# Performance work log

Measured on AMD Instinct MI355X. Metric: run time of the kernel, lower is better.

The kernel has to match this reference:

```python
import jax, jax.numpy as jnp
import numpy as np

B, T, I, H, O = 256, 2048, 6, 64, 6  # batch, time, input_dim, hidden_dim, output_dim


def setup_inputs() -> dict:
    key = jax.random.key(0)
    ks = jax.random.split(key, 11)
    s = 0.1  # param init scale
    return {
        "x": jax.random.normal(ks[0], (B, T, I), jnp.float32),
        # LSTM layer 0 (gate order i, f, g, o as in PyTorch; b = b_ih + b_hh)
        "Wih0": jax.random.normal(ks[1], (4 * H, I), jnp.float32) * s,
        "Whh0": jax.random.normal(ks[2], (4 * H, H), jnp.float32) * s,
        "b0": jax.random.normal(ks[3], (4 * H,), jnp.float32) * s,
        # LSTM layer 1
        "Wih1": jax.random.normal(ks[4], (4 * H, H), jnp.float32) * s,
        "Whh1": jax.random.normal(ks[5], (4 * H, H), jnp.float32) * s,
        "b1": jax.random.normal(ks[6], (4 * H,), jnp.float32) * s,
        # FC head
        "W1": jax.random.normal(ks[7], (H, H), jnp.float32) * s,
        "bf1": jax.random.normal(ks[8], (H,), jnp.float32) * s,
        "W2": jax.random.normal(ks[9], (O, H), jnp.float32) * s,
        "bf2": jax.random.normal(ks[10], (O,), jnp.float32) * s,
    }


def lstm_layer(x, Wih, Whh, b):
    """Single LSTM layer, batch_first. x: (B, T, F) -> (B, T, H)."""
    h_dim = Whh.shape[1]
    # precompute input contribution to gates for all timesteps: (B, T, 4H)
    xg = jnp.einsum('btf,gf->btg', x, Wih) + b

    def step(carry, xg_t):
        h, c = carry
        g = xg_t + h @ Whh.T                      # (B, 4H)
        i, f, gg, o = jnp.split(g, 4, axis=-1)    # PyTorch gate order i,f,g,o
        i = jax.nn.sigmoid(i)
        f = jax.nn.sigmoid(f)
        gg = jnp.tanh(gg)
        o = jax.nn.sigmoid(o)
        c = f * c + i * gg
        h = o * jnp.tanh(c)
        return (h, c), h

    h0 = jnp.zeros((x.shape[0], h_dim), x.dtype)
    _, hs = jax.lax.scan(step, (h0, h0), jnp.swapaxes(xg, 0, 1))  # (T, B, H)
    return jnp.swapaxes(hs, 0, 1)


def reference(x, Wih0, Whh0, b0, Wih1, Whh1, b1, W1, bf1, W2, bf2):
    h = lstm_layer(x, Wih0, Whh0, b0)
    h = lstm_layer(h, Wih1, Whh1, b1)   # eval mode: inter-layer dropout disabled
    h = jax.nn.relu(h @ W1.T + bf1)
    return h @ W2.T + bf2               # (B, T, O)
```

## Files before the change

### kernel.cpp

```cpp
#include <hip/hip_runtime.h>

#define TT 2048
#define HH 64
#define II 6
#define OO 6
#define NTHR 512

typedef float    f32x4 __attribute__((ext_vector_type(4)));
typedef _Float16 f16x8 __attribute__((ext_vector_type(8)));

__device__ __forceinline__ float fast_sig(float v) {
    return __builtin_amdgcn_rcpf(1.0f + __expf(-v));
}
__device__ __forceinline__ float fast_tanh(float v) {
    return 1.0f - 2.0f * __builtin_amdgcn_rcpf(__expf(2.0f * v) + 1.0f);
}

#define MFMA(a, b, c) __builtin_amdgcn_mfma_f32_16x16x32_f16((a), (b), (c), 0, 0, 0)

__global__
__attribute__((amdgpu_flat_work_group_size(NTHR, NTHR)))
__attribute__((amdgpu_waves_per_eu(2, 2)))
void lstm_mfma_kernel(const float* __restrict__ x,
                      const float* __restrict__ Wih0, const float* __restrict__ Whh0,
                      const float* __restrict__ b0,
                      const float* __restrict__ Wih1, const float* __restrict__ Whh1,
                      const float* __restrict__ b1,
                      const float* __restrict__ W1, const float* __restrict__ bf1,
                      const float* __restrict__ W2, const float* __restrict__ bf2,
                      float* __restrict__ out)
{
    const int row  = blockIdx.x;
    const int tid  = threadIdx.x;
    const int wid  = tid >> 6;
    const int lane = tid & 63;
    const int n    = lane & 15;
    const int q    = lane >> 4;
    const bool isA = wid < 4;
    const int  w   = isA ? wid : wid - 4;

    __shared__ __attribute__((aligned(16))) _Float16 H0[2][HH];
    __shared__ __attribute__((aligned(16))) _Float16 H1[2][HH];
    __shared__ __attribute__((aligned(16))) _Float16 Rb[2][HH];
    __shared__ __attribute__((aligned(16))) _Float16 Xb[2][32];
    __shared__ __attribute__((aligned(16))) float    XG[2][256];

    if (tid < HH) {
        H0[0][tid] = (_Float16)0.f; H0[1][tid] = (_Float16)0.f;
        H1[0][tid] = (_Float16)0.f; H1[1][tid] = (_Float16)0.f;
        Rb[0][tid] = (_Float16)0.f; Rb[1][tid] = (_Float16)0.f;
    }
    if (tid < 32) { Xb[0][tid] = (_Float16)0.f; Xb[1][tid] = (_Float16)0.f; }
    if (tid < 256) { XG[0][tid] = 0.f; XG[1][tid] = 0.f; }

    f16x8 frag[20];
    float bias[8];
    #pragma unroll
    for (int i = 0; i < 8; ++i) bias[i] = 0.f;

    auto mk = [&](const float* W, int r, int ld, int kbase, int kmax, bool rok) {
        f16x8 f;
        #pragma unroll
        for (int i = 0; i < 8; ++i) {
            int kk = kbase + 8 * q + i;
            f[i] = (rok && kk < kmax) ? (_Float16)W[r * ld + kk] : (_Float16)0.f;
        }
        return f;
    };

    if (isA) {
        #pragma unroll
        for (int g = 0; g < 4; ++g) {
            const int r0 = g * HH + 16 * w + n;
            frag[g * 3 + 0] = mk(Whh0, r0, HH, 0,  HH, true);
            frag[g * 3 + 1] = mk(Whh0, r0, HH, 32, HH, true);
            frag[g * 3 + 2] = mk(Wih0, r0, II, 0,  II, true);
            bias[g] = b0[r0];
            const int r1 = 16 * (4 * g + w) + n;
            frag[12 + g * 2 + 0] = mk(Wih1, r1, HH, 0,  HH, true);
            frag[12 + g * 2 + 1] = mk(Wih1, r1, HH, 32, HH, true);
            bias[4 + g] = b1[r1];
        }
    } else {
        #pragma unroll
        for (int g = 0; g < 4; ++g) {
            const int r0 = g * HH + 16 * w + n;
            frag[g * 2 + 0] = mk(Whh1, r0, HH, 0,  HH, true);
            frag[g * 2 + 1] = mk(Whh1, r0, HH, 32, HH, true);
        }
        const int rf = 16 * w + n;
        frag[8]  = mk(W1, rf, HH, 0,  HH, true);
        frag[9]  = mk(W1, rf, HH, 32, HH, true);
        bias[0] = bf1[rf];
        frag[10] = mk(W2, n, HH, 0,  HH, n < OO);
        frag[11] = mk(W2, n, HH, 32, HH, n < OO);
        bias[1] = (n < OO) ? bf2[n] : 0.f;
        #pragma unroll
        for (int i = 12; i < 20; ++i) frag[i] = frag[0];
    }

    const float* xrow   = x   + (size_t)row * TT * II;
    float*       outrow = out + (size_t)row * TT * OO;

    if (tid < II) Xb[0][tid] = (_Float16)xrow[tid];

    float cst = 0.f;
    __syncthreads();

    for (int t = 0; t <= TT + 3; ++t) {
        const int slp = (t + 1) & 1;
        const int slc = t & 1;

        if (isA) {
            const f16x8 a0 = *reinterpret_cast<const f16x8*>(&H0[slp][8 * q]);
            const f16x8 a1 = *reinterpret_cast<const f16x8*>(&H0[slp][32 + 8 * q]);
            const f16x8 a2 = *reinterpret_cast<const f16x8*>(&Xb[slc][8 * q]);
            f32x4 d0, d1, d2, d3;
            #pragma unroll
            for (int g = 0; g < 4; ++g) {
                f32x4 acc = {bias[g], bias[g], bias[g], bias[g]};
                acc = MFMA(a0, frag[g * 3 + 0], acc);
                acc = MFMA(a1, frag[g * 3 + 1], acc);
                acc = MFMA(a2, frag[g * 3 + 2], acc);
                if (g == 0) d0 = acc; else if (g == 1) d1 = acc;
                else if (g == 2) d2 = acc; else d3 = acc;
                f32x4 ae = {bias[4 + g], bias[4 + g], bias[4 + g], bias[4 + g]};
                ae = MFMA(a0, frag[12 + g * 2 + 0], ae);
                ae = MFMA(a1, frag[12 + g * 2 + 1], ae);
                if (lane < 16) XG[slp][16 * (4 * g + w) + lane] = ae[0];
            }
            if (t < TT) {
                float i_ = fast_sig(d0[0]), f_ = fast_sig(d1[0]);
                float g_ = fast_tanh(d2[0]), o_ = fast_sig(d3[0]);
                cst = f_ * cst + i_ * g_;
                float h = o_ * fast_tanh(cst);
                if (lane < 16) H0[slc][16 * w + lane] = (_Float16)h;
            }
            if (wid == 0 && lane < II && t + 1 < TT)
                Xb[slp][lane] = (_Float16)xrow[(size_t)(t + 1) * II + lane];
        } else {
            const int s2 = t - 2, s3 = t - 3, s4 = t - 4;
            const f16x8 a0 = *reinterpret_cast<const f16x8*>(&H1[slp][8 * q]);
            const f16x8 a1 = *reinterpret_cast<const f16x8*>(&H1[slp][32 + 8 * q]);
            f32x4 d0, d1, d2, d3;
            #pragma unroll
            for (int g = 0; g < 4; ++g) {
                const float xg = XG[slc][16 * (4 * g + w) + n];
                f32x4 acc = {xg, xg, xg, xg};
                acc = MFMA(a0, frag[g * 2 + 0], acc);
                acc = MFMA(a1, frag[g * 2 + 1], acc);
                if (g == 0) d0 = acc; else if (g == 1) d1 = acc;
                else if (g == 2) d2 = acc; else d3 = acc;
            }
            if (s2 >= 0 && s2 < TT) {
                float i_ = fast_sig(d0[0]), f_ = fast_sig(d1[0]);
                float g_ = fast_tanh(d2[0]), o_ = fast_sig(d3[0]);
                cst = f_ * cst + i_ * g_;
                float h = o_ * fast_tanh(cst);
                if (lane < 16) H1[slc][16 * w + lane] = (_Float16)h;
            }
            {
                f32x4 acc = {bias[0], bias[0], bias[0], bias[0]};
                acc = MFMA(a0, frag[8], acc);
                acc = MFMA(a1, frag[9], acc);
                if (s3 >= 0 && s3 < TT && lane < 16)
                    Rb[slp][16 * w + lane] = (_Float16)fmaxf(acc[0], 0.f);
            }
            if (w == 0) {
                const f16x8 r0 = *reinterpret_cast<const f16x8*>(&Rb[slc][8 * q]);
                const f16x8 r1 = *reinterpret_cast<const f16x8*>(&Rb[slc][32 + 8 * q]);
                f32x4 acc = {bias[1], bias[1], bias[1], bias[1]};
                acc = MFMA(r0, frag[10], acc);
                acc = MFMA(r1, frag[11], acc);
                if (s4 >= 0 && s4 < TT && lane < OO)
                    outrow[(size_t)s4 * OO + lane] = acc[0];
            }
        }
        __syncthreads();
    }
}

extern "C" void kernel_launch(void* const* d_in, const int* in_sizes, int n_in,
                              void* d_out, int out_size, void* d_ws, size_t ws_size,
                              hipStream_t stream) {
    const float* xp   = (const float*)d_in[0];
    const float* Wih0 = (const float*)d_in[1];
    const float* Whh0 = (const float*)d_in[2];
    const float* b0   = (const float*)d_in[3];
    const float* Wih1 = (const float*)d_in[4];
    const float* Whh1 = (const float*)d_in[5];
    const float* b1   = (const float*)d_in[6];
    const float* W1   = (const float*)d_in[7];
    const float* bf1  = (const float*)d_in[8];
    const float* W2   = (const float*)d_in[9];
    const float* bf2  = (const float*)d_in[10];
    float* outp = (float*)d_out;

    lstm_mfma_kernel<<<dim3(256), dim3(NTHR), 0, stream>>>(
        xp, Wih0, Whh0, b0, Wih1, Whh1, b1, W1, bf1, W2, bf2, outp);
}
```

Before: 1.215 ms.

## Batch 16 rows per block and split LSTM layers across producer/consumer blocks

Replaces the one-row-per-block kernel with 32 blocks: 16 producer blocks run layer 0 for 16 batch rows each and stream h0 through a global ring buffer to 16 consumer blocks that run layer 1 and the FC head. Batching 16 rows fills the MFMA N dimension instead of wasting 15 of 16 columns, and splitting the layers makes each block's per-step critical path shorter. Input projections are computed one step ahead by separate waves. The cost is cross-block spin-wait synchronization through global atomics, a memset of the workspace, and only 32 blocks on the device, so per-step latency dominates.

```diff
diff --git a/kernel.cpp b/kernel.cpp
--- a/kernel.cpp
+++ b/kernel.cpp
@@ -4,10 +4,16 @@
 #define HH 64
 #define II 6
 #define OO 6
+#define MB 16
+#define NG 16
+#define RING 256
 #define NTHR 512
 
 typedef float    f32x4 __attribute__((ext_vector_type(4)));
+typedef float    f32x2 __attribute__((ext_vector_type(2)));
 typedef _Float16 f16x8 __attribute__((ext_vector_type(8)));
+typedef _Float16 f16x4 __attribute__((ext_vector_type(4)));
+typedef _Float16 f16x2 __attribute__((ext_vector_type(2)));
 
 __device__ __forceinline__ float fast_sig(float v) {
     return __builtin_amdgcn_rcpf(1.0f + __expf(-v));
@@ -17,46 +23,47 @@
 }
 
 #define MFMA(a, b, c) __builtin_amdgcn_mfma_f32_16x16x32_f16((a), (b), (c), 0, 0, 0)
+#define LGKM_BARRIER() asm volatile("s_waitcnt lgkmcnt(0)\ns_barrier" ::: "memory")
 
 __global__
 __attribute__((amdgpu_flat_work_group_size(NTHR, NTHR)))
 __attribute__((amdgpu_waves_per_eu(2, 2)))
-void lstm_mfma_kernel(const float* __restrict__ x,
+void lstm_pipe_kernel(const float* __restrict__ x,
                       const float* __restrict__ Wih0, const float* __restrict__ Whh0,
                       const float* __restrict__ b0,
                       const float* __restrict__ Wih1, const float* __restrict__ Whh1,
                       const float* __restrict__ b1,
                       const float* __restrict__ W1, const float* __restrict__ bf1,
                       const float* __restrict__ W2, const float* __restrict__ bf2,
-                      float* __restrict__ out)
+                      float* __restrict__ out, void* __restrict__ ws)
 {
-    const int row  = blockIdx.x;
+    const int bid  = blockIdx.x;
+    const bool isP = bid < NG;
+    const int g    = isP ? bid : bid - NG;
+    const int row0 = g * MB;
     const int tid  = threadIdx.x;
     const int wid  = tid >> 6;
     const int lane = tid & 63;
     const int n    = lane & 15;
     const int q    = lane >> 4;
-    const bool isA = wid < 4;
-    const int  w   = isA ? wid : wid - 4;
-
-    __shared__ __attribute__((aligned(16))) _Float16 H0[2][HH];
-    __shared__ __attribute__((aligned(16))) _Float16 H1[2][HH];
-    __shared__ __attribute__((aligned(16))) _Float16 Rb[2][HH];
-    __shared__ __attribute__((aligned(16))) _Float16 Xb[2][32];
-    __shared__ __attribute__((aligned(16))) float    XG[2][256];
-
-    if (tid < HH) {
-        H0[0][tid] = (_Float16)0.f; H0[1][tid] = (_Float16)0.f;
-        H1[0][tid] = (_Float16)0.f; H1[1][tid] = (_Float16)0.f;
-        Rb[0][tid] = (_Float16)0.f; Rb[1][tid] = (_Float16)0.f;
-    }
-    if (tid < 32) { Xb[0][tid] = (_Float16)0.f; Xb[1][tid] = (_Float16)0.f; }
-    if (tid < 256) { XG[0][tid] = 0.f; XG[1][tid] = 0.f; }
-
-    f16x8 frag[20];
-    float bias[8];
-    #pragma unroll
-    for (int i = 0; i < 8; ++i) bias[i] = 0.f;
+
+    int* p0p = (int*)ws + (size_t)g * 64;
+    int* c0p = (int*)ws + (size_t)(NG + g) * 64;
+    _Float16* ring = (_Float16*)((char*)ws + 65536) + (size_t)g * (RING * 1024);
+
+    __shared__ __attribute__((aligned(16))) _Float16 H0 [4][1024];
+    __shared__ __attribute__((aligned(16))) _Float16 XT [2][128];
+    __shared__ __attribute__((aligned(16))) float    XG0[2][4][4][64][4];
+    __shared__ __attribute__((aligned(16))) _Float16 H0G[4][1024];
+    __shared__ __attribute__((aligned(16))) _Float16 H1 [2][1024];
+    __shared__ __attribute__((aligned(16))) _Float16 Rb [2][1024];
+    __shared__ __attribute__((aligned(16))) float    XG1[2][4][4][64][4];
+
+    for (int i = tid; i < 4 * 1024; i += NTHR) { H0[0][i] = (_Float16)0.f;
+                                                 H0G[0][i] = (_Float16)0.f; }
+    for (int i = tid; i < 2 * 1024; i += NTHR) { H1[0][i] = (_Float16)0.f;
+                                                 Rb[0][i]  = (_Float16)0.f; }
+    if (tid < 2 * 128) XT[0][tid] = (_Float16)0.f;
 
     auto mk = [&](const float* W, int r, int ld, int kbase, int kmax, bool rok) {
         f16x8 f;
@@ -67,116 +74,295 @@
         }
         return f;
     };
-
-    if (isA) {
+    const f32x4 zero4 = {0.f, 0.f, 0.f, 0.f};
+    f16x8 zero8;
+    #pragma unroll
+    for (int i = 0; i < 8; ++i) zero8[i] = (_Float16)0.f;
+
+    f16x8 FR[16];
+    f32x4 B[8];
+    #pragma unroll
+    for (int i = 0; i < 16; ++i) FR[i] = zero8;
+    #pragma unroll
+    for (int i = 0; i < 8; ++i) B[i] = zero4;
+
+    if (isP) {
+        if (wid < 4) {
+            #pragma unroll
+            for (int gg = 0; gg < 4; ++gg) {
+                const int r0 = gg * HH + 16 * wid + n;
+                FR[2 * gg + 0] = mk(Whh0, r0, HH, 0,  HH, true);
+                FR[2 * gg + 1] = mk(Whh0, r0, HH, 32, HH, true);
+            }
+        } else if (wid < 6) {
+            const int j = wid - 4;
+            #pragma unroll
+            for (int ti = 0; ti < 2; ++ti)
+                #pragma unroll
+                for (int gg = 0; gg < 4; ++gg) {
+                    const int tau = 2 * j + ti;
+                    FR[ti * 4 + gg] = mk(Wih0, gg * HH + 16 * tau + n, II, 0, II, true);
+                    const int u0 = gg * HH + 16 * tau + 4 * q;
+                    B[ti * 4 + gg] = f32x4{b0[u0], b0[u0+1], b0[u0+2], b0[u0+3]};
+                }
+        }
+    } else {
+        if (wid < 4) {
+            #pragma unroll
+            for (int gg = 0; gg < 4; ++gg) {
+                const int r0 = gg * HH + 16 * wid + n;
+                FR[2 * gg + 0] = mk(Whh1, r0, HH, 0,  HH, true);
+                FR[2 * gg + 1] = mk(Whh1, r0, HH, 32, HH, true);
+            }
+        } else if (wid < 6) {
+            const int j = wid - 4;
+            #pragma unroll
+            for (int ti = 0; ti < 2; ++ti)
+                #pragma unroll
+                for (int gg = 0; gg < 4; ++gg) {
+                    const int tau = 2 * j + ti;
+                    const int r0 = gg * HH + 16 * tau + n;
+                    FR[(ti * 4 + gg) * 2 + 0] = mk(Wih1, r0, HH, 0,  HH, true);
+                    FR[(ti * 4 + gg) * 2 + 1] = mk(Wih1, r0, HH, 32, HH, true);
+                    const int u0 = gg * HH + 16 * tau + 4 * q;
+                    B[ti * 4 + gg] = f32x4{b1[u0], b1[u0+1], b1[u0+2], b1[u0+3]};
+                }
+        } else if (wid == 7) {
+            #pragma unroll
+            for (int tau = 0; tau < 4; ++tau) {
+                FR[2 * tau + 0] = mk(W1, 16 * tau + n, HH, 0,  HH, true);
+                FR[2 * tau + 1] = mk(W1, 16 * tau + n, HH, 32, HH, true);
+                const int u0 = 16 * tau + 4 * q;
+                B[tau] = f32x4{bf1[u0], bf1[u0+1], bf1[u0+2], bf1[u0+3]};
+            }
+            FR[8] = mk(W2, n, HH, 0,  HH, n < OO);
+            FR[9] = mk(W2, n, HH, 32, HH, n < OO);
+            #pragma unroll
+            for (int r2 = 0; r2 < 4; ++r2) {
+                const int u = 4 * q + r2;
+                B[4][r2] = (u < OO) ? bf2[u] : 0.f;
+            }
+        }
+    }
+
+    const float* xs = nullptr;
+    if (isP && wid == 6 && lane < MB) {
+        const float* p = x + (size_t)(row0 + lane) * TT * II;
+        unsigned long long pp = (unsigned long long)p;
+        asm volatile("" : "+v"(pp));
+        xs = (const float*)pp;
+        f32x2 u0 = *(const f32x2*)(xs + II + 0);
+        f32x2 u1 = *(const f32x2*)(xs + II + 2);
+        f32x2 u2 = *(const f32x2*)(xs + II + 4);
+        *(f16x4*)&XT[1][lane * 8] = f16x4{(_Float16)u0[0], (_Float16)u0[1],
+                                          (_Float16)u1[0], (_Float16)u1[1]};
+        *(f16x2*)&XT[1][lane * 8 + 4] = f16x2{(_Float16)u2[0], (_Float16)u2[1]};
+    }
+    if (isP && (wid == 4 || wid == 5)) {
+        const int j = wid - 4;
+        f16x8 xb = zero8;
+        if (q == 0) {
+            const float* xp = x + (size_t)(row0 + n) * TT * II;
+            f32x2 a = *(const f32x2*)(xp + 0);
+            f32x2 b = *(const f32x2*)(xp + 2);
+            f32x2 c = *(const f32x2*)(xp + 4);
+            xb = f16x8{(_Float16)a[0], (_Float16)a[1], (_Float16)b[0], (_Float16)b[1],
+                       (_Float16)c[0], (_Float16)c[1], (_Float16)0.f, (_Float16)0.f};
+        }
         #pragma unroll
-        for (int g = 0; g < 4; ++g) {
-            const int r0 = g * HH + 16 * w + n;
-            frag[g * 3 + 0] = mk(Whh0, r0, HH, 0,  HH, true);
-            frag[g * 3 + 1] = mk(Whh0, r0, HH, 32, HH, true);
-            frag[g * 3 + 2] = mk(Wih0, r0, II, 0,  II, true);
-            bias[g] = b0[r0];
-            const int r1 = 16 * (4 * g + w) + n;
-            frag[12 + g * 2 + 0] = mk(Wih1, r1, HH, 0,  HH, true);
-            frag[12 + g * 2 + 1] = mk(Wih1, r1, HH, 32, HH, true);
-            bias[4 + g] = b1[r1];
-        }
-    } else {
+        for (int ti = 0; ti < 2; ++ti)
+            #pragma unroll
+            for (int gg = 0; gg < 4; ++gg) {
+                f32x4 acc = MFMA(FR[ti * 4 + gg], xb, B[ti * 4 + gg]);
+                *(f32x4*)&XG0[0][2 * j + ti][gg][lane][0] = acc;
+            }
+    }
+
+    auto cellact = [&](const f32x4& d0, const f32x4& d1, const f32x4& d2,
+                       const f32x4& d3, f32x4& cs) {
+        f16x4 hh;
         #pragma unroll
-        for (int g = 0; g < 4; ++g) {
-            const int r0 = g * HH + 16 * w + n;
-            frag[g * 2 + 0] = mk(Whh1, r0, HH, 0,  HH, true);
-            frag[g * 2 + 1] = mk(Whh1, r0, HH, 32, HH, true);
-        }
-        const int rf = 16 * w + n;
-        frag[8]  = mk(W1, rf, HH, 0,  HH, true);
-        frag[9]  = mk(W1, rf, HH, 32, HH, true);
-        bias[0] = bf1[rf];
-        frag[10] = mk(W2, n, HH, 0,  HH, n < OO);
-        frag[11] = mk(W2, n, HH, 32, HH, n < OO);
-        bias[1] = (n < OO) ? bf2[n] : 0.f;
-        #pragma unroll
-        for (int i = 12; i < 20; ++i) frag[i] = frag[0];
-    }
-
-    const float* xrow   = x   + (size_t)row * TT * II;
-    float*       outrow = out + (size_t)row * TT * OO;
-
-    if (tid < II) Xb[0][tid] = (_Float16)xrow[tid];
-
-    float cst = 0.f;
+        for (int r2 = 0; r2 < 4; ++r2) {
+            float i_ = fast_sig(d0[r2]), f_ = fast_sig(d1[r2]);
+            float g_ = fast_tanh(d2[r2]), o_ = fast_sig(d3[r2]);
+            cs[r2] = f_ * cs[r2] + i_ * g_;
+            hh[r2] = (_Float16)(o_ * fast_tanh(cs[r2]));
+        }
+        return hh;
+    };
+
+    f32x4 cst = zero4;
     __syncthreads();
 
-    for (int t = 0; t <= TT + 3; ++t) {
-        const int slp = (t + 1) & 1;
-        const int slc = t & 1;
-
-        if (isA) {
-            const f16x8 a0 = *reinterpret_cast<const f16x8*>(&H0[slp][8 * q]);
-            const f16x8 a1 = *reinterpret_cast<const f16x8*>(&H0[slp][32 + 8 * q]);
-            const f16x8 a2 = *reinterpret_cast<const f16x8*>(&Xb[slc][8 * q]);
-            f32x4 d0, d1, d2, d3;
-            #pragma unroll
-            for (int g = 0; g < 4; ++g) {
-                f32x4 acc = {bias[g], bias[g], bias[g], bias[g]};
-                acc = MFMA(a0, frag[g * 3 + 0], acc);
-                acc = MFMA(a1, frag[g * 3 + 1], acc);
-                acc = MFMA(a2, frag[g * 3 + 2], acc);
-                if (g == 0) d0 = acc; else if (g == 1) d1 = acc;
-                else if (g == 2) d2 = acc; else d3 = acc;
-                f32x4 ae = {bias[4 + g], bias[4 + g], bias[4 + g], bias[4 + g]};
-                ae = MFMA(a0, frag[12 + g * 2 + 0], ae);
-                ae = MFMA(a1, frag[12 + g * 2 + 1], ae);
-                if (lane < 16) XG[slp][16 * (4 * g + w) + lane] = ae[0];
-            }
-            if (t < TT) {
-                float i_ = fast_sig(d0[0]), f_ = fast_sig(d1[0]);
-                float g_ = fast_tanh(d2[0]), o_ = fast_sig(d3[0]);
-                cst = f_ * cst + i_ * g_;
-                float h = o_ * fast_tanh(cst);
-                if (lane < 16) H0[slc][16 * w + lane] = (_Float16)h;
-            }
-            if (wid == 0 && lane < II && t + 1 < TT)
-                Xb[slp][lane] = (_Float16)xrow[(size_t)(t + 1) * II + lane];
+    const int EMAX = isP ? TT : TT + 4;
+    for (int e = 0; e <= EMAX; ++e) {
+        if (isP) {
+            if (wid < 4) {
+                const f16x8 a0 = *(const f16x8*)&H0[(e + 3) & 3][q * 128 + n * 8];
+                const f16x8 a1 = *(const f16x8*)&H0[(e + 3) & 3][512 + q * 128 + n * 8];
+                f32x4 d0, d1, d2, d3;
+                #pragma unroll
+                for (int gg = 0; gg < 4; ++gg) {
+                    f32x4 xg = *(const f32x4*)&XG0[e & 1][wid][gg][lane][0];
+                    f32x4 pA = MFMA(FR[2 * gg + 0], a0, xg);
+                    f32x4 pB = MFMA(FR[2 * gg + 1], a1, zero4);
+                    f32x4 d = pA + pB;
+                    if (gg == 0) d0 = d; else if (gg == 1) d1 = d;
+                    else if (gg == 2) d2 = d; else d3 = d;
+                }
+                if (e < TT) {
+                    f16x4 hh = cellact(d0, d1, d2, d3, cst);
+                    *(f16x4*)&H0[e & 3][(2 * wid + (q >> 1)) * 128 + n * 8 + (q & 1) * 4] = hh;
+                }
+            } else if (wid < 6) {
+                if (e + 1 < TT) {
+                    const int j = wid - 4;
+                    f16x8 xb = zero8;
+                    if (q == 0) xb = *(const f16x8*)&XT[(e + 1) & 1][n * 8];
+                    #pragma unroll
+                    for (int ti = 0; ti < 2; ++ti)
+                        #pragma unroll
+                        for (int gg = 0; gg < 4; ++gg) {
+                            f32x4 acc = MFMA(FR[ti * 4 + gg], xb, B[ti * 4 + gg]);
+                            *(f32x4*)&XG0[(e + 1) & 1][2 * j + ti][gg][lane][0] = acc;
+                        }
+                }
+            } else if (wid == 6) {
+                if (lane < MB && e + 2 < TT) {
+                    const float* xp2 = xs + (size_t)(e + 2) * II;
+                    f32x2 u0 = *(const f32x2*)(xp2 + 0);
+                    f32x2 u1 = *(const f32x2*)(xp2 + 2);
+                    f32x2 u2 = *(const f32x2*)(xp2 + 4);
+                    *(f16x4*)&XT[e & 1][lane * 8] =
+                        f16x4{(_Float16)u0[0], (_Float16)u0[1],
+                              (_Float16)u1[0], (_Float16)u1[1]};
+                    *(f16x2*)&XT[e & 1][lane * 8 + 4] =
+                        f16x2{(_Float16)u2[0], (_Float16)u2[1]};
+                }
+            } else {
+                if ((e & 1) == 0 && e >= 2) {
+                    #pragma unroll
+                    for (int d = 2; d >= 1; --d) {
+                        const int m = e - d;
+                        if (m >= 0 && m < TT) {
+                            f16x8 v0 = *(const f16x8*)&H0[m & 3][lane * 16];
+                            f16x8 v1 = *(const f16x8*)&H0[m & 3][lane * 16 + 8];
+                            _Float16* dst = ring + (size_t)(m & (RING - 1)) * 1024 + lane * 16;
+                            *(f16x8*)dst = v0;
+                            *(f16x8*)(dst + 8) = v1;
+                        }
+                    }
+                    asm volatile("s_waitcnt vmcnt(0)" ::: "memory");
+                    __threadfence();
+                    if (lane == 0)
+                        __hip_atomic_store(p0p, e, __ATOMIC_RELEASE,
+                                           __HIP_MEMORY_SCOPE_AGENT);
+                    if (lane == 0 && e >= RING - 64 && (e & 63) == 0) {
+                        while (__hip_atomic_load(c0p, __ATOMIC_RELAXED,
+                                                 __HIP_MEMORY_SCOPE_AGENT)
+                               < e - (RING - 64))
+                            __builtin_amdgcn_s_sleep(8);
+                    }
+                }
+            }
         } else {
-            const int s2 = t - 2, s3 = t - 3, s4 = t - 4;
-            const f16x8 a0 = *reinterpret_cast<const f16x8*>(&H1[slp][8 * q]);
-            const f16x8 a1 = *reinterpret_cast<const f16x8*>(&H1[slp][32 + 8 * q]);
-            f32x4 d0, d1, d2, d3;
-            #pragma unroll
-            for (int g = 0; g < 4; ++g) {
-                const float xg = XG[slc][16 * (4 * g + w) + n];
-                f32x4 acc = {xg, xg, xg, xg};
-                acc = MFMA(a0, frag[g * 2 + 0], acc);
-                acc = MFMA(a1, frag[g * 2 + 1], acc);
-                if (g == 0) d0 = acc; else if (g == 1) d1 = acc;
-                else if (g == 2) d2 = acc; else d3 = acc;
-            }
-            if (s2 >= 0 && s2 < TT) {
-                float i_ = fast_sig(d0[0]), f_ = fast_sig(d1[0]);
-                float g_ = fast_tanh(d2[0]), o_ = fast_sig(d3[0]);
-                cst = f_ * cst + i_ * g_;
-                float h = o_ * fast_tanh(cst);
-                if (lane < 16) H1[slc][16 * w + lane] = (_Float16)h;
-            }
-            {
-                f32x4 acc = {bias[0], bias[0], bias[0], bias[0]};
-                acc = MFMA(a0, frag[8], acc);
-                acc = MFMA(a1, frag[9], acc);
-                if (s3 >= 0 && s3 < TT && lane < 16)
-                    Rb[slp][16 * w + lane] = (_Float16)fmaxf(acc[0], 0.f);
-            }
-            if (w == 0) {
-                const f16x8 r0 = *reinterpret_cast<const f16x8*>(&Rb[slc][8 * q]);
-                const f16x8 r1 = *reinterpret_cast<const f16x8*>(&Rb[slc][32 + 8 * q]);
-                f32x4 acc = {bias[1], bias[1], bias[1], bias[1]};
-                acc = MFMA(r0, frag[10], acc);
-                acc = MFMA(r1, frag[11], acc);
-                if (s4 >= 0 && s4 < TT && lane < OO)
-                    outrow[(size_t)s4 * OO + lane] = acc[0];
-            }
-        }
-        __syncthreads();
+            if (wid < 4) {
+                const int u = e - 3;
+                const f16x8 a0 = *(const f16x8*)&H1[e & 1][q * 128 + n * 8];
+                const f16x8 a1 = *(const f16x8*)&H1[e & 1][512 + q * 128 + n * 8];
+                f32x4 d0, d1, d2, d3;
+                #pragma unroll
+                for (int gg = 0; gg < 4; ++gg) {
+                    f32x4 xg = *(const f32x4*)&XG1[(e + 1) & 1][wid][gg][lane][0];
+                    f32x4 pA = MFMA(FR[2 * gg + 0], a0, xg);
+                    f32x4 pB = MFMA(FR[2 * gg + 1], a1, zero4);
+                    f32x4 d = pA + pB;
+                    if (gg == 0) d0 = d; else if (gg == 1) d1 = d;
+                    else if (gg == 2) d2 = d; else d3 = d;
+                }
+                if (u >= 0 && u < TT) {
+                    f16x4 hh = cellact(d0, d1, d2, d3, cst);
+                    *(f16x4*)&H1[(e + 1) & 1][(2 * wid + (q >> 1)) * 128 + n * 8 + (q & 1) * 4] = hh;
+                }
+            } else if (wid < 6) {
+                const int m2 = e - 2;
+                if (m2 >= 0 && m2 < TT) {
+                    const int j = wid - 4;
+                    const f16x8 h0a = *(const f16x8*)&H0G[m2 & 3][q * 128 + n * 8];
+                    const f16x8 h0b = *(const f16x8*)&H0G[m2 & 3][512 + q * 128 + n * 8];
+                    #pragma unroll
+                    for (int ti = 0; ti < 2; ++ti)
+                        #pragma unroll
+                        for (int gg = 0; gg < 4; ++gg) {
+                            f32x4 acc = MFMA(FR[(ti * 4 + gg) * 2 + 0], h0a, B[ti * 4 + gg]);
+                            f32x4 ac2 = MFMA(FR[(ti * 4 + gg) * 2 + 1], h0b, zero4);
+                            *(f32x4*)&XG1[m2 & 1][2 * j + ti][gg][lane][0] = acc + ac2;
+                        }
+                }
+            } else if (wid == 6) {
+                if ((e & 1) == 0) {
+                    const int mHi = (e < TT) ? e : TT - 1;
+                    if (mHi >= 0 && e - 1 < TT) {
+                        int pv = 0;
+                        if (lane == 0) {
+                            pv = __hip_atomic_load(p0p, __ATOMIC_RELAXED,
+                                                   __HIP_MEMORY_SCOPE_AGENT);
+                            while (pv < mHi + 1) {
+                                __builtin_amdgcn_s_sleep(8);
+                                pv = __hip_atomic_load(p0p, __ATOMIC_RELAXED,
+                                                       __HIP_MEMORY_SCOPE_AGENT);
+                            }
+                        }
+                        __threadfence();
+                        #pragma unroll
+                        for (int d = 1; d >= 0; --d) {
+                            const int m = e - d;
+                            if (m >= 0 && m < TT) {
+                                const _Float16* src =
+                                    ring + (size_t)(m & (RING - 1)) * 1024 + lane * 16;
+                                f16x8 v0 = *(const f16x8*)src;
+                                f16x8 v1 = *(const f16x8*)(src + 8);
+                                *(f16x8*)&H0G[m & 3][lane * 16] = v0;
+                                *(f16x8*)&H0G[m & 3][lane * 16 + 8] = v1;
+                            }
+                        }
+                    }
+                    if (lane == 0 && (e & 63) == 0)
+                        __hip_atomic_store(c0p, e, __ATOMIC_RELAXED,
+                                           __HIP_MEMORY_SCOPE_AGENT);
+                }
+            } else {
+                const int v = e - 4, v2 = e - 5;
+                const f16x8 b0f = *(const f16x8*)&H1[e & 1][q * 128 + n * 8];
+                const f16x8 b1f = *(const f16x8*)&H1[e & 1][512 + q * 128 + n * 8];
+                #pragma unroll
+                for (int tau = 0; tau < 4; ++tau) {
+                    f32x4 acc = MFMA(FR[2 * tau + 0], b0f, B[tau]);
+                    f32x4 ac2 = MFMA(FR[2 * tau + 1], b1f, zero4);
+                    f32x4 fv = acc + ac2;
+                    if (v >= 0 && v < TT) {
+                        f16x4 rv = {(_Float16)fmaxf(fv[0], 0.f), (_Float16)fmaxf(fv[1], 0.f),
+                                    (_Float16)fmaxf(fv[2], 0.f), (_Float16)fmaxf(fv[3], 0.f)};
+                        *(f16x4*)&Rb[e & 1][(2 * tau + (q >> 1)) * 128 + n * 8 + (q & 1) * 4] = rv;
+                    }
+                }
+                const f16x8 r0 = *(const f16x8*)&Rb[(e + 1) & 1][q * 128 + n * 8];
+                const f16x8 r1 = *(const f16x8*)&Rb[(e + 1) & 1][512 + q * 128 + n * 8];
+                f32x4 o0 = MFMA(FR[8], r0, B[4]);
+                f32x4 o1 = MFMA(FR[9], r1, zero4);
+                f32x4 ov = o0 + o1;
+                if (v2 >= 0 && v2 < TT) {
+                    float* po = out + (size_t)(row0 + n) * TT * OO + (size_t)v2 * OO;
+                    if (q == 0) {
+                        *(f32x2*)(po + 0) = f32x2{ov[0], ov[1]};
+                        *(f32x2*)(po + 2) = f32x2{ov[2], ov[3]};
+                    } else if (q == 1) {
+                        *(f32x2*)(po + 4) = f32x2{ov[0], ov[1]};
+                    }
+                }
+            }
+        }
+        LGKM_BARRIER();
     }
 }
 
@@ -196,6 +382,7 @@
     const float* bf2  = (const float*)d_in[10];
     float* outp = (float*)d_out;
 
-    lstm_mfma_kernel<<<dim3(256), dim3(NTHR), 0, stream>>>(
-        xp, Wih0, Whh0, b0, Wih1, Whh1, b1, W1, bf1, W2, bf2, outp);
+    hipMemsetAsync(d_ws, 0, 65536, stream);
+    lstm_pipe_kernel<<<dim3(2 * NG), dim3(NTHR), 0, stream>>>(
+        xp, Wih0, Whh0, b0, Wih1, Whh1, b1, W1, bf1, W2, bf2, outp, d_ws);
 }
```

Result: slower. 2.132 ms (+75.5%).
